# Optimization experiments

Measured on AMD Instinct MI355X. Metric: run time of the kernel, lower is better.

Reference implementation:

```python
import jax, jax.numpy as jnp
import numpy as np
from jax.scipy.special import ndtr

# ---- constants matching init_kwargs ----
DF = 4.0            # fixed_df (closed-form Student-t4 quantile used)
EWMA_ALPHA = 0.94
SCALE_EPS = 1e-5
T_STEPS = 50        # diff_steps
BETA_START = 1e-4
BETA_END = 0.1
L = 6               # residual_layers
C = 32              # residual_channels
EMB = 512           # diffusion step-embedding width


def _t4_ppf(u):
    """Exact Student-t(df=4) quantile (Shaw closed form); u in (0,1)."""
    a = jnp.clip(4.0 * u * (1.0 - u), 1e-12, 1.0)
    r = jnp.sqrt(a)
    q = 2.0 * jnp.sqrt(jnp.maximum(jnp.cos(jnp.arccos(r) / 3.0) / r - 1.0, 0.0))
    return jnp.sign(u - 0.5) * q


def _forward(x_hist, z_init, noise, w_in, b_in, temb_w1, temb_b1, temb_w2, temb_b2,
             lyr_wt, lyr_bt, lyr_wdil, lyr_bdil, lyr_wout, lyr_bout,
             w_o1, b_o1, w_o2, b_o2, num_samples):
    B, Tc, D = x_hist.shape
    S = num_samples
    # ---- Student-t marginal fit (EWMA variance recurrence as lax.scan) ----
    loc = jnp.mean(x_hist, axis=1, keepdims=True)              # [B,1,D]
    c2 = (x_hist - loc) ** 2                                    # [B,Tc,D]
    def ewma_step(v, c):
        return EWMA_ALPHA * v + (1.0 - EWMA_ALPHA) * c, None
    v_last, _ = jax.lax.scan(ewma_step, c2[:, 0, :], jnp.swapaxes(c2[:, 1:, :], 0, 1))
    scale_f = jnp.maximum(jnp.sqrt(v_last * (DF - 2.0) / DF), SCALE_EPS)  # [B,D]

    # ---- DDPM schedule (linear betas) ----
    betas = jnp.linspace(BETA_START, BETA_END, T_STEPS).astype(jnp.float32)
    alphas = 1.0 - betas
    abar = jnp.cumprod(alphas)
    abar_prev = jnp.concatenate([jnp.ones((1,), jnp.float32), abar[:-1]])
    coef_x0 = betas * jnp.sqrt(abar_prev) / (1.0 - abar)
    coef_xt = (1.0 - abar_prev) * jnp.sqrt(alphas) / (1.0 - abar)
    post_var = betas * (1.0 - abar_prev) / (1.0 - abar)
    sqrt_ab = jnp.sqrt(abar)
    sqrt_1mab = jnp.sqrt(1.0 - abar)

    half = jnp.arange(64, dtype=jnp.float32)

    def eps_net(x, t):
        # diffusion-step embedding
        e = t.astype(jnp.float32) * 10.0 ** (half * 4.0 / 63.0)
        pe = jnp.concatenate([jnp.sin(e), jnp.cos(e)])          # [128]
        te = jax.nn.silu(pe @ temb_w1 + temb_b1)
        te = jax.nn.silu(te @ temb_w2 + temb_b2)                # [EMB]
        h = jax.nn.relu(jnp.einsum('cd,bdh->bch', w_in, x) + b_in[:, None])
        skip = jnp.zeros_like(h)
        for i in range(L):
            cond = te @ lyr_wt[i] + lyr_bt[i]                   # [C]
            d = 2 ** i
            y = jax.lax.conv_general_dilated(
                h + cond[None, :, None], lyr_wdil[i], (1,), [(d, d)],
                rhs_dilation=(d,), dimension_numbers=('NCH', 'OIH', 'NCH')
            ) + lyr_bdil[i][None, :, None]                       # [B,2C,H]
            gate, filt = jnp.split(y, 2, axis=1)
            y = jnp.tanh(filt) * jax.nn.sigmoid(gate)            # [B,C,H]
            y = jnp.einsum('oc,bch->boh', lyr_wout[i], y) + lyr_bout[i][None, :, None]
            res, sk = jnp.split(y, 2, axis=1)
            h = (h + res) * (1.0 / np.sqrt(2.0))
            skip = skip + sk
        s = jax.nn.relu(jnp.einsum('oc,bch->boh', w_o1, skip * (1.0 / np.sqrt(L))) + b_o1[:, None])
        return jnp.einsum('dc,bch->bdh', w_o2, s) + b_o2[:, None]

    @jax.checkpoint
    def ddpm_step(x, inp):
        t, nz = inp
        eps = eps_net(x, t)
        x0 = jnp.clip((x - sqrt_1mab[t] * eps) / sqrt_ab[t], -1.0, 1.0)  # clip_denoised
        mean = coef_x0[t] * x0 + coef_xt[t] * x
        x = mean + jnp.where(t > 0, jnp.sqrt(post_var[t]), 0.0) * nz
        return x, None

    ts = jnp.arange(T_STEPS - 1, -1, -1)
    z, _ = jax.lax.scan(ddpm_step, z_init, (ts, noise))          # [S*B,D,H]
    H = z.shape[-1]
    z = z.reshape(S, B, D, H).transpose(0, 1, 3, 2)              # [S,B,H,D]

    # ---- Gaussian -> Student-t marginal transform ----
    u = jnp.clip(ndtr(z), 1e-6, 1.0 - 1e-6)
    t_std = _t4_ppf(u)
    return loc[None] + scale_f[None, :, None, :] * t_std          # [S,B,H,D]


def setup_inputs() -> dict:
    key = jax.random.key(0)
    ks = jax.random.split(key, 12)
    D, Tc, H, B, S = 128, 192, 24, 32, 16
    p = lambda k, sh: jax.random.normal(k, sh, jnp.float32) * 0.05
    z = lambda sh: jnp.zeros(sh, jnp.float32)
    return {
        'x_hist': jax.random.normal(ks[0], (B, Tc, D), jnp.float32),
        'z_init': jax.random.normal(ks[1], (S * B, D, H), jnp.float32),
        'noise': jax.random.normal(ks[2], (T_STEPS, S * B, D, H), jnp.float32),
        'w_in': p(ks[3], (C, D)), 'b_in': z((C,)),
        'temb_w1': p(ks[4], (128, EMB)), 'temb_b1': z((EMB,)),
        'temb_w2': p(ks[5], (EMB, EMB)), 'temb_b2': z((EMB,)),
        'lyr_wt': p(ks[6], (L, EMB, C)), 'lyr_bt': z((L, C)),
        'lyr_wdil': p(ks[7], (L, 2 * C, C, 3)), 'lyr_bdil': z((L, 2 * C)),
        'lyr_wout': p(ks[8], (L, 2 * C, C)), 'lyr_bout': z((L, 2 * C)),
        'w_o1': p(ks[9], (C, C)), 'b_o1': z((C,)),
        'w_o2': p(ks[10], (D, C)), 'b_o2': z((D,)),
        'num_samples': 16,
    }


def reference(x_hist, z_init, noise, w_in, b_in, temb_w1, temb_b1, temb_w2, temb_b2,
              lyr_wt, lyr_bt, lyr_wdil, lyr_bdil, lyr_wout, lyr_bout,
              w_o1, b_o1, w_o2, b_o2, num_samples):
    return _forward(x_hist, z_init, noise, w_in, b_in, temb_w1, temb_b1, temb_w2, temb_b2,
                    lyr_wt, lyr_bt, lyr_wdil, lyr_bdil, lyr_wout, lyr_bout,
                    w_o1, b_o1, w_o2, b_o2, num_samples)
```

## Files before the change

kernel.cpp:

```cpp
#include <hip/hip_runtime.h>
#include <math.h>

#define T_STEPS 50
#define NB 512
#define RS2 0.70710678118654752f
#define INV_SQRT_L 0.40824829046386302f
#define WPACK_SHORT_OFF 36864

struct SchedArg { float cx0[T_STEPS], cxt[T_STEPS], sig[T_STEPS], s1m[T_STEPS], isab[T_STEPS]; };
struct FreqArg  { double f[64]; };

typedef short bf16x8 __attribute__((ext_vector_type(8)));
typedef float f32x4  __attribute__((ext_vector_type(4)));

__device__ __forceinline__ float4 ld4s(const float* p) { return *reinterpret_cast<const float4*>(p); }
__device__ __forceinline__ void   st4s(float* p, float4 v) { *reinterpret_cast<float4*>(p) = v; }
__device__ __forceinline__ float4 ld4g(const float* __restrict__ p) { return *reinterpret_cast<const float4*>(p); }
__device__ __forceinline__ float fast_sig(float x)  { return 1.f / (1.f + __expf(-x)); }
__device__ __forceinline__ float fast_tanh(float x) { float e = __expf(2.f * x); return 1.f - 2.f / (e + 1.f); }

__device__ __forceinline__ unsigned rne1(float f) {
    unsigned u = __float_as_uint(f);
    return (u + 0x7FFFu + ((u >> 16) & 1u)) >> 16;
}
__device__ __forceinline__ unsigned pk2(float a, float b) {
    return (rne1(a) & 0xFFFFu) | (rne1(b) << 16);
}
__device__ __forceinline__ void st_bf4(short* p, float a, float b, float c, float d) {
    uint2 v; v.x = pk2(a, b); v.y = pk2(c, d);
    *reinterpret_cast<uint2*>(p) = v;
}
__device__ __forceinline__ float bf2f(unsigned hi16) {
    return __uint_as_float(hi16 << 16);
}
__device__ __forceinline__ f32x4 mma(bf16x8 a, bf16x8 b, f32x4 c) {
    return __builtin_amdgcn_mfma_f32_16x16x32_bf16(a, b, c, 0, 0, 0);
}
__device__ __forceinline__ f32x4 bias4s(const float* p) {
    float4 b = ld4s(p);
    f32x4 r; r[0] = b.x; r[1] = b.y; r[2] = b.z; r[3] = b.w;
    return r;
}
__device__ __forceinline__ bf16x8 ldfrag(const short* p) {
    return *reinterpret_cast<const bf16x8*>(p);
}

__global__ __launch_bounds__(256) void fit_kernel(const float* __restrict__ xh,
                                                  float* __restrict__ loc,
                                                  float* __restrict__ scalef) {
    int gid = blockIdx.x * 256 + threadIdx.x;
    int b = gid >> 7, d = gid & 127;
    const float* p = xh + (size_t)b * 192 * 128 + d;
    float s = 0.f;
    for (int t = 0; t < 192; ++t) s += p[t * 128];
    float m = s * (1.0f / 192.0f);
    float v = 0.f;
    for (int t = 0; t < 192; ++t) {
        float c = p[t * 128] - m; c *= c;
        v = (t == 0) ? c : 0.94f * v + (1.0f - 0.94f) * c;
    }
    loc[gid] = m;
    scalef[gid] = fmaxf(sqrtf(v * 0.5f), 1e-5f);
}

__global__ __launch_bounds__(256) void temb_kernel(
    const float* __restrict__ w1, const float* __restrict__ b1,
    const float* __restrict__ w2, const float* __restrict__ b2,
    const float* __restrict__ wt, const float* __restrict__ bt,
    float* __restrict__ cond_all, FreqArg fq) {
    int t = blockIdx.x;
    int tid = threadIdx.x;
    __shared__ float pe[128], te1[512], te2[512];
    if (tid < 64) {
        double e = (double)t * fq.f[tid];
        pe[tid]      = (float)sin(e);
        pe[tid + 64] = (float)cos(e);
    }
    __syncthreads();
    for (int j = tid; j < 512; j += 256) {
        float acc = b1[j];
        for (int k = 0; k < 128; ++k) acc += pe[k] * w1[k * 512 + j];
        te1[j] = acc / (1.f + expf(-acc));
    }
    __syncthreads();
    for (int j = tid; j < 512; j += 256) {
        float acc = b2[j];
        for (int k = 0; k < 512; ++k) acc += te1[k] * w2[k * 512 + j];
        te2[j] = acc / (1.f + expf(-acc));
    }
    __syncthreads();
    if (tid < 192) {
        int l = tid >> 5, c = tid & 31;
        float acc = bt[l * 32 + c];
        const float* w = wt + (size_t)l * 512 * 32 + c;
        for (int k = 0; k < 512; ++k) acc += te2[k] * w[k * 32];
        cond_all[t * 192 + tid] = acc;
    }
}

__global__ __launch_bounds__(256) void prep_kernel(
    const float* __restrict__ w_in, const float* __restrict__ lyr_wdil,
    const float* __restrict__ lyr_wout, const float* __restrict__ w_o1,
    const float* __restrict__ w_o2, short* __restrict__ wpack) {
    int gid = blockIdx.x * 256 + threadIdx.x;
    if (gid >= 58368) return;
    int j = gid & 7, l = (gid >> 3) & 63, frag = gid >> 9;
    int m = l & 15, k = (l >> 4) * 8 + j;
    float v;
    if (frag < 8) {
        int m2 = frag >> 2, ks = frag & 3;
        v = w_in[(m2 * 16 + m) * 128 + ks * 32 + k];
    } else if (frag < 80) {
        int fi = frag - 8;
        int li = fi / 12, rem = fi % 12;
        int mg = rem / 6, rem2 = rem % 6;
        int tp = rem2 >> 1, gf = rem2 & 1;
        int o = gf * 32 + mg * 16 + m;
        v = lyr_wdil[((li * 64 + o) * 32 + k) * 3 + tp];
    } else if (frag < 104) {
        int fi = frag - 80;
        int li = fi >> 2, mo = fi & 3;
        v = lyr_wout[li * 2048 + (mo * 16 + m) * 32 + k];
    } else if (frag < 106) {
        int m2 = frag - 104;
        v = w_o1[(m2 * 16 + m) * 32 + k] * INV_SQRT_L;
    } else {
        int m8 = frag - 106;
        v = w_o2[(m8 * 16 + m) * 32 + k];
    }
    wpack[gid] = (short)rne1(v);
}

__global__ __launch_bounds__(256, 2) void diffusion_kernel(
    const float* __restrict__ z_init, const float* __restrict__ noise,
    const float* __restrict__ b_in,  const float* __restrict__ lyr_bdil,
    const float* __restrict__ lyr_bout, const float* __restrict__ b_o1,
    const float* __restrict__ b_o2, const float* __restrict__ cond_all,
    const short* __restrict__ wpack, const float* __restrict__ loc,
    const float* __restrict__ scalef, float* __restrict__ out, SchedArg sc) {

    __shared__ __align__(16) float xsf[24 * 132];
    __shared__ __align__(16) short xbB[32 * 136];
    __shared__ __align__(16) short hB [32 * 40];
    __shared__ __align__(16) short hcB[33 * 40];
    __shared__ __align__(16) short actB[32 * 40];
    __shared__ __align__(16) short skB[32 * 40];
    __shared__ __align__(16) float biasB[960];
    __shared__ __align__(16) float condB[2][192];

    const int tid = threadIdx.x;
    const int wv  = __builtin_amdgcn_readfirstlane(tid >> 6);
    const int l   = tid & 63;
    const int ln  = l & 15;
    const int lq  = l >> 4;
    const int bb  = blockIdx.x;

    const short* wpP1 = wpack;
    const short* wpCv = wpack + 4096;
    const short* wpWo = wpack + 40960;
    const short* wpO1 = wpack + 53248;
    const short* wpO2 = wpack + 54272;

    const int m2   = wv >> 1;
    const int nn   = wv & 1;
    const int colw = nn * 16 + ln;
    const bool cvw = (colw < 24);

    bf16x8 aP1[4], aCv[6][3][2], aO1, aWo[6], aO2[2];
#pragma unroll
    for (int ks = 0; ks < 4; ++ks)
        aP1[ks] = ldfrag(wpP1 + (m2 * 4 + ks) * 512 + l * 8);
    aO1 = ldfrag(wpO1 + m2 * 512 + l * 8);
#pragma unroll
    for (int li = 0; li < 6; ++li) {
#pragma unroll
        for (int tp = 0; tp < 3; ++tp) {
            if (li == 5 && tp != 1) continue;
#pragma unroll
            for (int gf = 0; gf < 2; ++gf)
                aCv[li][tp][gf] = ldfrag(wpCv + (li * 12 + m2 * 6 + tp * 2 + gf) * 512 + l * 8);
        }
        aWo[li] = ldfrag(wpWo + (li * 4 + wv) * 512 + l * 8);
    }
    aO2[0] = ldfrag(wpO2 + wv * 512 + l * 8);
    aO2[1] = ldfrag(wpO2 + (wv + 4) * 512 + l * 8);

    for (int i = tid; i < 3072; i += 256) {
        int d = i / 24, h = i - d * 24;
        float v = z_init[(size_t)bb * 3072 + i];
        xsf[h * 132 + d] = v;
        xbB[h * 136 + d] = (short)rne1(v);
    }
    for (int i = tid; i < 1088; i += 256) xbB[24 * 136 + i] = 0;
    for (int i = tid; i < 960; i += 256) {
        float v;
        if      (i < 32)  v = b_in[i];
        else if (i < 416) v = lyr_bdil[i - 32];
        else if (i < 800) v = lyr_bout[i - 416];
        else if (i < 832) v = b_o1[i - 800];
        else              v = b_o2[i - 832];
        biasB[i] = v;
    }
    if (tid < 192) condB[0][tid] = cond_all[(T_STEPS - 1) * 192 + tid];
    if (tid < 40) hcB[32 * 40 + tid] = 0;
    for (int i = tid; i < 640; i += 256) reinterpret_cast<unsigned*>(skB)[i] = 0u;
    __syncthreads();

    for (int step = 0; step < T_STEPS; ++step) {
        const int t = T_STEPS - 1 - step;
        const float* cnd = condB[step & 1];

        float cndnext = 0.f;
        if (step + 1 < T_STEPS && tid < 192)
            cndnext = cond_all[(t - 1) * 192 + tid];

        {
            f32x4 acc = bias4s(biasB + m2 * 16 + lq * 4);
            const short* xb = xbB + colw * 136;
#pragma unroll
            for (int ks = 0; ks < 4; ++ks)
                acc = mma(aP1[ks], ldfrag(xb + ks * 32 + lq * 8), acc);
            float h0 = fmaxf(acc[0], 0.f), h1 = fmaxf(acc[1], 0.f);
            float h2 = fmaxf(acc[2], 0.f), h3 = fmaxf(acc[3], 0.f);
            float4 cv = ld4s(cnd + m2 * 16 + lq * 4);
            st_bf4(hB + colw * 40 + m2 * 16 + lq * 4, h0, h1, h2, h3);
            st_bf4(hcB + colw * 40 + m2 * 16 + lq * 4,
                   h0 + cv.x, h1 + cv.y, h2 + cv.z, h3 + cv.w);
        }
        __syncthreads();

#pragma unroll
        for (int li = 0; li < 6; ++li) {
            const int dd = 1 << li;
            {
                f32x4 accg = bias4s(biasB + 32 + li * 64 + m2 * 16 + lq * 4);
                f32x4 accf = bias4s(biasB + 32 + li * 64 + 32 + m2 * 16 + lq * 4);
#pragma unroll
                for (int tp = 0; tp < 3; ++tp) {
                    if (li == 5 && tp != 1) continue;
                    int hh = colw + (tp - 1) * dd;
                    int colp = ((unsigned)hh < 24u) ? hh : 32;
                    bf16x8 b = ldfrag(hcB + colp * 40 + lq * 8);
                    accg = mma(aCv[li][tp][0], b, accg);
                    accf = mma(aCv[li][tp][1], b, accf);
                }
                st_bf4(actB + colw * 40 + m2 * 16 + lq * 4,
                       fast_tanh(accf[0]) * fast_sig(accg[0]),
                       fast_tanh(accf[1]) * fast_sig(accg[1]),
                       fast_tanh(accf[2]) * fast_sig(accg[2]),
                       fast_tanh(accf[3]) * fast_sig(accg[3]));
            }
            __syncthreads();

            {
                const int mo = wv;
                if (!(li == 5 && mo < 2)) {
                    f32x4 bo = bias4s(biasB + 416 + li * 64 + mo * 16 + lq * 4);
#pragma unroll
                    for (int n = 0; n < 2; ++n) {
                        const int col = n * 16 + ln;
                        f32x4 acc = mma(aWo[li], ldfrag(actB + col * 40 + lq * 8), bo);
                        if (mo < 2) {
                            short* hp = hB + col * 40 + mo * 16 + lq * 4;
                            uint2 hv = *reinterpret_cast<uint2*>(hp);
                            float n0 = (bf2f(hv.x & 0xFFFFu) + acc[0]) * RS2;
                            float n1 = (bf2f(hv.x >> 16)     + acc[1]) * RS2;
                            float n2 = (bf2f(hv.y & 0xFFFFu) + acc[2]) * RS2;
                            float n3 = (bf2f(hv.y >> 16)     + acc[3]) * RS2;
                            st_bf4(hp, n0, n1, n2, n3);
                            float4 cv = ld4s(cnd + (li + 1) * 32 + mo * 16 + lq * 4);
                            st_bf4(hcB + col * 40 + mo * 16 + lq * 4,
                                   n0 + cv.x, n1 + cv.y, n2 + cv.z, n3 + cv.w);
                        } else {
                            short* sp = skB + col * 40 + (mo - 2) * 16 + lq * 4;
                            uint2 sv = *reinterpret_cast<uint2*>(sp);
                            st_bf4(sp,
                                   bf2f(sv.x & 0xFFFFu) + acc[0],
                                   bf2f(sv.x >> 16)     + acc[1],
                                   bf2f(sv.y & 0xFFFFu) + acc[2],
                                   bf2f(sv.y >> 16)     + acc[3]);
                        }
                    }
                }
            }
            __syncthreads();
        }

        {
            f32x4 acc = bias4s(biasB + 800 + m2 * 16 + lq * 4);
            acc = mma(aO1, ldfrag(skB + colw * 40 + lq * 8), acc);
            st_bf4(actB + colw * 40 + m2 * 16 + lq * 4,
                   fmaxf(acc[0], 0.f), fmaxf(acc[1], 0.f),
                   fmaxf(acc[2], 0.f), fmaxf(acc[3], 0.f));
        }
        __syncthreads();

        {
            const float cx0 = sc.cx0[t], cxt = sc.cxt[t], sig = sc.sig[t];
            const float s1m = sc.s1m[t], isab = sc.isab[t];
#pragma unroll
            for (int mi = 0; mi < 2; ++mi) {
                const int d0 = (wv + 4 * mi) * 16 + lq * 4;
                f32x4 bia = bias4s(biasB + 832 + d0);
#pragma unroll
                for (int n = 0; n < 2; ++n) {
                    const int col = n * 16 + ln;
                    f32x4 acc = mma(aO2[mi], ldfrag(actB + col * 40 + lq * 8), bia);
                    if (col < 24) {
                        float* xp = xsf + col * 132 + d0;
                        float4 xv = ld4s(xp);
                        const float* nzp = noise + ((size_t)step * NB + bb) * 3072 + col;
                        float4 rr;
#pragma unroll
                        for (int i = 0; i < 4; ++i) {
                            float xvv = (&xv.x)[i];
                            float nz = nzp[(d0 + i) * 24];
                            float x0 = fminf(fmaxf((xvv - s1m * acc[i]) * isab, -1.f), 1.f);
                            (&rr.x)[i] = cx0 * x0 + cxt * xvv + sig * nz;
                        }
                        st4s(xp, rr);
                        st_bf4(xbB + col * 136 + d0, rr.x, rr.y, rr.z, rr.w);
                    }
                }
            }
            for (int i = tid; i < 640; i += 256) reinterpret_cast<unsigned*>(skB)[i] = 0u;
            if (step + 1 < T_STEPS && tid < 192)
                condB[(step + 1) & 1][tid] = cndnext;
        }
        __syncthreads();
    }

    {
        const int b = bb & 31;
        for (int i = tid; i < 768; i += 256) {
            int col = i >> 5, q = i & 31;
            float4 zv = ld4s(xsf + col * 132 + q * 4);
            float4 l4 = ld4g(loc + b * 128 + q * 4);
            float4 s4 = ld4g(scalef + b * 128 + q * 4);
            float4 o4;
#pragma unroll
            for (int e = 0; e < 4; ++e) {
                float u = 0.5f * (1.f + erff((&zv.x)[e] * RS2));
                u = fminf(fmaxf(u, 1e-6f), 1.f - 1e-6f);
                float a4 = fminf(fmaxf(4.f * u * (1.f - u), 1e-12f), 1.f);
                float rr = sqrtf(a4);
                float q2 = 2.f * sqrtf(fmaxf(cosf(acosf(rr) * (1.f / 3.f)) / rr - 1.f, 0.f));
                float tstd = (u < 0.5f) ? -q2 : q2;
                (&o4.x)[e] = (&l4.x)[e] + (&s4.x)[e] * tstd;
            }
            *reinterpret_cast<float4*>(out + ((size_t)bb * 24 + col) * 128 + q * 4) = o4;
        }
    }
}

extern "C" void kernel_launch(void* const* d_in, const int* in_sizes, int n_in,
                              void* d_out, int out_size, void* d_ws, size_t ws_size,
                              hipStream_t stream) {
    const float* x_hist  = (const float*)d_in[0];
    const float* z_init  = (const float*)d_in[1];
    const float* noise   = (const float*)d_in[2];
    const float* w_in    = (const float*)d_in[3];
    const float* b_in    = (const float*)d_in[4];
    const float* temb_w1 = (const float*)d_in[5];
    const float* temb_b1 = (const float*)d_in[6];
    const float* temb_w2 = (const float*)d_in[7];
    const float* temb_b2 = (const float*)d_in[8];
    const float* lyr_wt  = (const float*)d_in[9];
    const float* lyr_bt  = (const float*)d_in[10];
    const float* lyr_wdil= (const float*)d_in[11];
    const float* lyr_bdil= (const float*)d_in[12];
    const float* lyr_wout= (const float*)d_in[13];
    const float* lyr_bout= (const float*)d_in[14];
    const float* w_o1    = (const float*)d_in[15];
    const float* b_o1    = (const float*)d_in[16];
    const float* w_o2    = (const float*)d_in[17];
    const float* b_o2    = (const float*)d_in[18];
    float* out = (float*)d_out;

    float* loc      = (float*)d_ws;
    float* scalef   = loc + 4096;
    float* cond_all = scalef + 4096;
    short* wpack    = (short*)d_ws + WPACK_SHORT_OFF;

    SchedArg sa;
    double abar = 1.0;
    for (int t = 0; t < T_STEPS; ++t) {
        double beta  = 1e-4 + (0.1 - 1e-4) * ((double)t / 49.0);
        double alpha = 1.0 - beta;
        double abprev = abar;
        abar *= alpha;
        sa.cx0[t]  = (float)(beta * sqrt(abprev) / (1.0 - abar));
        sa.cxt[t]  = (float)((1.0 - abprev) * sqrt(alpha) / (1.0 - abar));
        double pv  = beta * (1.0 - abprev) / (1.0 - abar);
        sa.sig[t]  = (t > 0) ? (float)sqrt(pv) : 0.f;
        sa.s1m[t]  = (float)sqrt(1.0 - abar);
        sa.isab[t] = (float)(1.0 / sqrt(abar));
    }
    FreqArg fa;
    for (int j = 0; j < 64; ++j) fa.f[j] = pow(10.0, (double)j * 4.0 / 63.0);

    prep_kernel<<<228, 256, 0, stream>>>(w_in, lyr_wdil, lyr_wout, w_o1, w_o2, wpack);
    fit_kernel<<<16, 256, 0, stream>>>(x_hist, loc, scalef);
    temb_kernel<<<T_STEPS, 256, 0, stream>>>(temb_w1, temb_b1, temb_w2, temb_b2,
                                             lyr_wt, lyr_bt, cond_all, fa);
    diffusion_kernel<<<NB, 256, 0, stream>>>(z_init, noise, b_in, lyr_bdil,
                                             lyr_bout, b_o1, b_o2, cond_all,
                                             wpack, loc, scalef, out, sa);
}
```

Baseline: 525.9 us.

## Keep residual, skip, and sample state in registers; use hardware bf16 pack

Moves the residual stream h, the skip accumulator and the fp32 sample state x out of shared memory into per-lane registers. The output-projection weights are split so each wave computes both the residual and skip fragments for its own tile. This removes the shared-memory read-modify-write of hB and skB, the per-step skB zeroing, and the xsf array. It also swaps the software round-to-nearest bf16 packing for the v_cvt_pk_bf16_f32 instruction. The cost is higher register pressure under launch_bounds(256,2), which risks spills or a drop in occupancy.

Result: faster. 488.2 us (-7.2%).

```diff
diff --git a/kernel.cpp b/kernel.cpp
--- a/kernel.cpp
+++ b/kernel.cpp
@@ -24,14 +24,13 @@
     return (u + 0x7FFFu + ((u >> 16) & 1u)) >> 16;
 }
 __device__ __forceinline__ unsigned pk2(float a, float b) {
-    return (rne1(a) & 0xFFFFu) | (rne1(b) << 16);
+    unsigned r;
+    asm("v_cvt_pk_bf16_f32 %0, %1, %2" : "=v"(r) : "v"(a), "v"(b));
+    return r;
 }
 __device__ __forceinline__ void st_bf4(short* p, float a, float b, float c, float d) {
     uint2 v; v.x = pk2(a, b); v.y = pk2(c, d);
     *reinterpret_cast<uint2*>(p) = v;
-}
-__device__ __forceinline__ float bf2f(unsigned hi16) {
-    return __uint_as_float(hi16 << 16);
 }
 __device__ __forceinline__ f32x4 mma(bf16x8 a, bf16x8 b, f32x4 c) {
     return __builtin_amdgcn_mfma_f32_16x16x32_bf16(a, b, c, 0, 0, 0);
@@ -139,9 +138,7 @@
     const short* __restrict__ wpack, const float* __restrict__ loc,
     const float* __restrict__ scalef, float* __restrict__ out, SchedArg sc) {
 
-    __shared__ __align__(16) float xsf[24 * 132];
     __shared__ __align__(16) short xbB[32 * 136];
-    __shared__ __align__(16) short hB [32 * 40];
     __shared__ __align__(16) short hcB[33 * 40];
     __shared__ __align__(16) short actB[32 * 40];
     __shared__ __align__(16) short skB[32 * 40];
@@ -161,16 +158,16 @@
     const short* wpO1 = wpack + 53248;
     const short* wpO2 = wpack + 54272;
 
-    const int m2   = wv >> 1;
+    const int mh   = wv >> 1;
     const int nn   = wv & 1;
     const int colw = nn * 16 + ln;
     const bool cvw = (colw < 24);
 
-    bf16x8 aP1[4], aCv[6][3][2], aO1, aWo[6], aO2[2];
+    bf16x8 aP1[4], aCv[6][3][2], aO1, aWoR[5], aWoS[6], aO2[2];
 #pragma unroll
     for (int ks = 0; ks < 4; ++ks)
-        aP1[ks] = ldfrag(wpP1 + (m2 * 4 + ks) * 512 + l * 8);
-    aO1 = ldfrag(wpO1 + m2 * 512 + l * 8);
+        aP1[ks] = ldfrag(wpP1 + (mh * 4 + ks) * 512 + l * 8);
+    aO1 = ldfrag(wpO1 + mh * 512 + l * 8);
 #pragma unroll
     for (int li = 0; li < 6; ++li) {
 #pragma unroll
@@ -178,18 +175,17 @@
             if (li == 5 && tp != 1) continue;
 #pragma unroll
             for (int gf = 0; gf < 2; ++gf)
-                aCv[li][tp][gf] = ldfrag(wpCv + (li * 12 + m2 * 6 + tp * 2 + gf) * 512 + l * 8);
-        }
-        aWo[li] = ldfrag(wpWo + (li * 4 + wv) * 512 + l * 8);
+                aCv[li][tp][gf] = ldfrag(wpCv + (li * 12 + mh * 6 + tp * 2 + gf) * 512 + l * 8);
+        }
+        if (li < 5) aWoR[li] = ldfrag(wpWo + (li * 4 + mh) * 512 + l * 8);
+        aWoS[li] = ldfrag(wpWo + (li * 4 + 2 + mh) * 512 + l * 8);
     }
     aO2[0] = ldfrag(wpO2 + wv * 512 + l * 8);
     aO2[1] = ldfrag(wpO2 + (wv + 4) * 512 + l * 8);
 
     for (int i = tid; i < 3072; i += 256) {
         int d = i / 24, h = i - d * 24;
-        float v = z_init[(size_t)bb * 3072 + i];
-        xsf[h * 132 + d] = v;
-        xbB[h * 136 + d] = (short)rne1(v);
+        xbB[h * 136 + d] = (short)rne1(z_init[(size_t)bb * 3072 + i]);
     }
     for (int i = tid; i < 1088; i += 256) xbB[24 * 136 + i] = 0;
     for (int i = tid; i < 960; i += 256) {
@@ -203,7 +199,18 @@
     }
     if (tid < 192) condB[0][tid] = cond_all[(T_STEPS - 1) * 192 + tid];
     if (tid < 40) hcB[32 * 40 + tid] = 0;
-    for (int i = tid; i < 640; i += 256) reinterpret_cast<unsigned*>(skB)[i] = 0u;
+
+    f32x4 xr[2][2];
+#pragma unroll
+    for (int mi = 0; mi < 2; ++mi)
+#pragma unroll
+        for (int n = 0; n < 2; ++n) {
+            const int col = n * 16 + ln;
+            const int d0 = (wv + 4 * mi) * 16 + lq * 4;
+#pragma unroll
+            for (int i = 0; i < 4; ++i)
+                xr[mi][n][i] = (col < 24) ? z_init[(size_t)bb * 3072 + (d0 + i) * 24 + col] : 0.f;
+        }
     __syncthreads();
 
     for (int step = 0; step < T_STEPS; ++step) {
@@ -214,27 +221,31 @@
         if (step + 1 < T_STEPS && tid < 192)
             cndnext = cond_all[(t - 1) * 192 + tid];
 
+        f32x4 hr;
         {
-            f32x4 acc = bias4s(biasB + m2 * 16 + lq * 4);
+            f32x4 acc = bias4s(biasB + mh * 16 + lq * 4);
             const short* xb = xbB + colw * 136;
 #pragma unroll
             for (int ks = 0; ks < 4; ++ks)
                 acc = mma(aP1[ks], ldfrag(xb + ks * 32 + lq * 8), acc);
-            float h0 = fmaxf(acc[0], 0.f), h1 = fmaxf(acc[1], 0.f);
-            float h2 = fmaxf(acc[2], 0.f), h3 = fmaxf(acc[3], 0.f);
-            float4 cv = ld4s(cnd + m2 * 16 + lq * 4);
-            st_bf4(hB + colw * 40 + m2 * 16 + lq * 4, h0, h1, h2, h3);
-            st_bf4(hcB + colw * 40 + m2 * 16 + lq * 4,
-                   h0 + cv.x, h1 + cv.y, h2 + cv.z, h3 + cv.w);
-        }
+#pragma unroll
+            for (int i = 0; i < 4; ++i) acc[i] = fmaxf(acc[i], 0.f);
+            hr = acc;
+            float4 cv = ld4s(cnd + mh * 16 + lq * 4);
+            st_bf4(hcB + colw * 40 + mh * 16 + lq * 4,
+                   hr[0] + cv.x, hr[1] + cv.y, hr[2] + cv.z, hr[3] + cv.w);
+        }
+        f32x4 skr;
+#pragma unroll
+        for (int i = 0; i < 4; ++i) skr[i] = 0.f;
         __syncthreads();
 
 #pragma unroll
         for (int li = 0; li < 6; ++li) {
             const int dd = 1 << li;
             {
-                f32x4 accg = bias4s(biasB + 32 + li * 64 + m2 * 16 + lq * 4);
-                f32x4 accf = bias4s(biasB + 32 + li * 64 + 32 + m2 * 16 + lq * 4);
+                f32x4 accg = bias4s(biasB + 32 + li * 64 + mh * 16 + lq * 4);
+                f32x4 accf = bias4s(biasB + 32 + li * 64 + 32 + mh * 16 + lq * 4);
 #pragma unroll
                 for (int tp = 0; tp < 3; ++tp) {
                     if (li == 5 && tp != 1) continue;
@@ -244,7 +255,7 @@
                     accg = mma(aCv[li][tp][0], b, accg);
                     accf = mma(aCv[li][tp][1], b, accf);
                 }
-                st_bf4(actB + colw * 40 + m2 * 16 + lq * 4,
+                st_bf4(actB + colw * 40 + mh * 16 + lq * 4,
                        fast_tanh(accf[0]) * fast_sig(accg[0]),
                        fast_tanh(accf[1]) * fast_sig(accg[1]),
                        fast_tanh(accf[2]) * fast_sig(accg[2]),
@@ -253,43 +264,31 @@
             __syncthreads();
 
             {
-                const int mo = wv;
-                if (!(li == 5 && mo < 2)) {
-                    f32x4 bo = bias4s(biasB + 416 + li * 64 + mo * 16 + lq * 4);
-#pragma unroll
-                    for (int n = 0; n < 2; ++n) {
-                        const int col = n * 16 + ln;
-                        f32x4 acc = mma(aWo[li], ldfrag(actB + col * 40 + lq * 8), bo);
-                        if (mo < 2) {
-                            short* hp = hB + col * 40 + mo * 16 + lq * 4;
-                            uint2 hv = *reinterpret_cast<uint2*>(hp);
-                            float n0 = (bf2f(hv.x & 0xFFFFu) + acc[0]) * RS2;
-                            float n1 = (bf2f(hv.x >> 16)     + acc[1]) * RS2;
-                            float n2 = (bf2f(hv.y & 0xFFFFu) + acc[2]) * RS2;
-                            float n3 = (bf2f(hv.y >> 16)     + acc[3]) * RS2;
-                            st_bf4(hp, n0, n1, n2, n3);
-                            float4 cv = ld4s(cnd + (li + 1) * 32 + mo * 16 + lq * 4);
-                            st_bf4(hcB + col * 40 + mo * 16 + lq * 4,
-                                   n0 + cv.x, n1 + cv.y, n2 + cv.z, n3 + cv.w);
-                        } else {
-                            short* sp = skB + col * 40 + (mo - 2) * 16 + lq * 4;
-                            uint2 sv = *reinterpret_cast<uint2*>(sp);
-                            st_bf4(sp,
-                                   bf2f(sv.x & 0xFFFFu) + acc[0],
-                                   bf2f(sv.x >> 16)     + acc[1],
-                                   bf2f(sv.y & 0xFFFFu) + acc[2],
-                                   bf2f(sv.y >> 16)     + acc[3]);
-                        }
-                    }
+                bf16x8 b = ldfrag(actB + colw * 40 + lq * 8);
+                if (li < 5) {
+                    f32x4 accR = mma(aWoR[li], b,
+                                     bias4s(biasB + 416 + li * 64 + mh * 16 + lq * 4));
+#pragma unroll
+                    for (int i = 0; i < 4; ++i) hr[i] = (hr[i] + accR[i]) * RS2;
+                    float4 cv = ld4s(cnd + (li + 1) * 32 + mh * 16 + lq * 4);
+                    st_bf4(hcB + colw * 40 + mh * 16 + lq * 4,
+                           hr[0] + cv.x, hr[1] + cv.y, hr[2] + cv.z, hr[3] + cv.w);
                 }
+                f32x4 accS = mma(aWoS[li], b,
+                                 bias4s(biasB + 416 + li * 64 + (2 + mh) * 16 + lq * 4));
+#pragma unroll
+                for (int i = 0; i < 4; ++i) skr[i] += accS[i];
+                if (li == 5)
+                    st_bf4(skB + colw * 40 + mh * 16 + lq * 4,
+                           skr[0], skr[1], skr[2], skr[3]);
             }
             __syncthreads();
         }
 
         {
-            f32x4 acc = bias4s(biasB + 800 + m2 * 16 + lq * 4);
+            f32x4 acc = bias4s(biasB + 800 + mh * 16 + lq * 4);
             acc = mma(aO1, ldfrag(skB + colw * 40 + lq * 8), acc);
-            st_bf4(actB + colw * 40 + m2 * 16 + lq * 4,
+            st_bf4(actB + colw * 40 + mh * 16 + lq * 4,
                    fmaxf(acc[0], 0.f), fmaxf(acc[1], 0.f),
                    fmaxf(acc[2], 0.f), fmaxf(acc[3], 0.f));
         }
@@ -307,23 +306,20 @@
                     const int col = n * 16 + ln;
                     f32x4 acc = mma(aO2[mi], ldfrag(actB + col * 40 + lq * 8), bia);
                     if (col < 24) {
-                        float* xp = xsf + col * 132 + d0;
-                        float4 xv = ld4s(xp);
                         const float* nzp = noise + ((size_t)step * NB + bb) * 3072 + col;
-                        float4 rr;
+                        float xn[4];
 #pragma unroll
                         for (int i = 0; i < 4; ++i) {
-                            float xvv = (&xv.x)[i];
+                            float xv = xr[mi][n][i];
                             float nz = nzp[(d0 + i) * 24];
-                            float x0 = fminf(fmaxf((xvv - s1m * acc[i]) * isab, -1.f), 1.f);
-                            (&rr.x)[i] = cx0 * x0 + cxt * xvv + sig * nz;
+                            float x0 = fminf(fmaxf((xv - s1m * acc[i]) * isab, -1.f), 1.f);
+                            xn[i] = cx0 * x0 + cxt * xv + sig * nz;
+                            xr[mi][n][i] = xn[i];
                         }
-                        st4s(xp, rr);
-                        st_bf4(xbB + col * 136 + d0, rr.x, rr.y, rr.z, rr.w);
+                        st_bf4(xbB + col * 136 + d0, xn[0], xn[1], xn[2], xn[3]);
                     }
                 }
             }
-            for (int i = tid; i < 640; i += 256) reinterpret_cast<unsigned*>(skB)[i] = 0u;
             if (step + 1 < T_STEPS && tid < 192)
                 condB[(step + 1) & 1][tid] = cndnext;
         }
@@ -332,23 +328,29 @@
 
     {
         const int b = bb & 31;
-        for (int i = tid; i < 768; i += 256) {
-            int col = i >> 5, q = i & 31;
-            float4 zv = ld4s(xsf + col * 132 + q * 4);
-            float4 l4 = ld4g(loc + b * 128 + q * 4);
-            float4 s4 = ld4g(scalef + b * 128 + q * 4);
-            float4 o4;
-#pragma unroll
-            for (int e = 0; e < 4; ++e) {
-                float u = 0.5f * (1.f + erff((&zv.x)[e] * RS2));
-                u = fminf(fmaxf(u, 1e-6f), 1.f - 1e-6f);
-                float a4 = fminf(fmaxf(4.f * u * (1.f - u), 1e-12f), 1.f);
-                float rr = sqrtf(a4);
-                float q2 = 2.f * sqrtf(fmaxf(cosf(acosf(rr) * (1.f / 3.f)) / rr - 1.f, 0.f));
-                float tstd = (u < 0.5f) ? -q2 : q2;
-                (&o4.x)[e] = (&l4.x)[e] + (&s4.x)[e] * tstd;
+#pragma unroll
+        for (int mi = 0; mi < 2; ++mi) {
+#pragma unroll
+            for (int n = 0; n < 2; ++n) {
+                const int col = n * 16 + ln;
+                if (col >= 24) continue;
+                const int d0 = (wv + 4 * mi) * 16 + lq * 4;
+                float4 l4 = ld4g(loc + b * 128 + d0);
+                float4 s4 = ld4g(scalef + b * 128 + d0);
+                float4 o4;
+#pragma unroll
+                for (int e = 0; e < 4; ++e) {
+                    float z = xr[mi][n][e];
+                    float u = 0.5f * (1.f + erff(z * RS2));
+                    u = fminf(fmaxf(u, 1e-6f), 1.f - 1e-6f);
+                    float a4 = fminf(fmaxf(4.f * u * (1.f - u), 1e-12f), 1.f);
+                    float rr = sqrtf(a4);
+                    float q2 = 2.f * sqrtf(fmaxf(cosf(acosf(rr) * (1.f / 3.f)) / rr - 1.f, 0.f));
+                    float tstd = (u < 0.5f) ? -q2 : q2;
+                    (&o4.x)[e] = (&l4.x)[e] + (&s4.x)[e] * tstd;
+                }
+                *reinterpret_cast<float4*>(out + (size_t)bb * 3072 + col * 128 + d0) = o4;
             }
-            *reinterpret_cast<float4*>(out + ((size_t)bb * 24 + col) * 128 + q * 4) = o4;
         }
     }
 }
```
